# Kernel tuning notes

Measured on AMD Instinct MI355X. Metric: run time of the kernel, lower is better.

Reference implementation:

```python
import jax, jax.numpy as jnp
import numpy as np

B, C, N, H = 4, 256, 1024, 8
D = C            # per-head q/k dim (out_channels defaults to in_channels)
DV = C           # per-head value/output dim (y_out_channels defaults to out_channels)


def setup_inputs() -> dict:
    key = jax.random.key(0)
    ks = jax.random.split(key, 10)
    s = 0.02
    return {
        "x": jax.random.normal(ks[0], (B, C, N), jnp.float32),
        "y": jax.random.normal(ks[1], (B, C, N), jnp.float32),
        "Wq": jax.random.normal(ks[2], (H * D, C), jnp.float32) * s,
        "bq": jnp.zeros((H * D,), jnp.float32),
        "Wk": jax.random.normal(ks[3], (H * D, C), jnp.float32) * s,
        "bk": jnp.zeros((H * D,), jnp.float32),
        "Wv": jax.random.normal(ks[4], (H * DV, C), jnp.float32) * s,
        "bv": jnp.zeros((H * DV,), jnp.float32),
        "Wp": jax.random.normal(ks[5], (DV, C), jnp.float32) * s,  # projection, bias=False
        "gamma": jax.random.uniform(ks[6], (H, 1, 1, 1), jnp.float32) + 0.001,
    }


def _pconv(t, W, b):
    # 1x1 conv1d: (O,C) x (B,C,N) -> (B,O,N)
    out = jnp.einsum('oc,bcn->bon', W, t)
    return out if b is None else out + b[None, :, None]


def reference(x, y, Wq, bq, Wk, bk, Wv, bv, Wp, gamma):
    b_, _, n_ = x.shape
    h = gamma.shape[0]
    # Q/K/V projections, split channels into h heads (head-major chunks of D)
    q = _pconv(x, Wq, bq).reshape(b_, h, -1, n_)   # [B,H,D,N]
    k = _pconv(x, Wk, bk).reshape(b_, h, -1, n_)   # [B,H,D,N]
    v = _pconv(y, Wv, bv).reshape(b_, h, -1, n_)   # [B,H,DV,N]
    # energy[i,j] = sum_d q[d,i]*k[d,j]; softmax over keys j (no sqrt(d) scaling)
    attn = jax.nn.softmax(jnp.einsum('bhdn,bhdm->bhnm', q, k), axis=-1)
    out = jnp.einsum('bhdm,bhnm->bhdn', v, attn)   # [B,H,DV,N]
    # residual branch: y projected to DV channels (1x1 conv, no bias)
    yp = jnp.einsum('oc,bcn->bon', Wp, y)          # [B,DV,N]
    g = gamma.reshape(1, h, 1, 1)
    out = (g * out + yp[:, None, :, :]) / (1.0 + g)
    # concat heads along channel dim (head-major), matching split_cat(out,1,0,2)
    return out.reshape(b_, -1, n_)                 # [B,H*DV,N]
```

## Files before the change

### kernel.cpp

```cpp
#include <hip/hip_runtime.h>

#define Bb 4
#define Cc 256
#define Nn 1024
#define Hh 8
#define Oo 2048

typedef __attribute__((ext_vector_type(8))) short bf16x8;
typedef __attribute__((ext_vector_type(4))) float f32x4;

__device__ __forceinline__ short f2bf(float f) {
  unsigned u = __builtin_bit_cast(unsigned, f);
  unsigned r = u + 0x7FFFu + ((u >> 16) & 1u);
  return (short)(r >> 16);
}
__device__ __forceinline__ f32x4 mfma16(bf16x8 a, bf16x8 b, f32x4 c) {
  return __builtin_amdgcn_mfma_f32_16x16x32_bf16(a, b, c, 0, 0, 0);
}
__device__ __forceinline__ void gl_lds16(const void* g, void* l) {
  __builtin_amdgcn_global_load_lds(
      (const __attribute__((address_space(1))) void*)g,
      (__attribute__((address_space(3))) void*)l, 16, 0, 0);
}

__device__ __forceinline__ void stage_row512(const char* gbase, char* lds,
                                             int wave, int lane) {
#pragma unroll
  for (int i = 0; i < 8; i++) {
    int off = (wave * 8 + i) * 1024;
    int L = off + lane * 16;
    int r = L >> 9;
    int c = ((L >> 4) & 31) ^ (r & 7);
    gl_lds16(gbase + r * 512 + c * 16, lds + off);
  }
}
__device__ __forceinline__ void stage_v(const char* Vg, char* lds, int k0,
                                        int wave, int lane) {
#pragma unroll
  for (int i = 0; i < 8; i++) {
    int off = (wave * 8 + i) * 1024;
    int L = off + lane * 16;
    int r = L >> 7;
    int c = ((L >> 4) & 7) ^ (r & 7);
    gl_lds16(Vg + (size_t)r * 2048 + k0 * 2 + c * 16, lds + off);
  }
}

__global__ __launch_bounds__(256) void k_transpose(
    const float* __restrict__ x, const float* __restrict__ y,
    short* __restrict__ xT, short* __restrict__ yT,
    const float* __restrict__ Wq, const float* __restrict__ Wk,
    const float* __restrict__ Wv, const float* __restrict__ Wp,
    short* __restrict__ dWq, short* __restrict__ dWk, short* __restrict__ dWv,
    short* __restrict__ dWp) {
  {
    const int NW = Oo * Cc;
    int lin = blockIdx.x + 16 * (blockIdx.y + 4 * blockIdx.z);
    for (int i = (lin * 256 + threadIdx.x) * 4; i < 3 * NW + Cc * Cc;
         i += 512 * 256 * 4) {
      const float* src;
      short* dst;
      int off;
      if (i < NW) {
        src = Wq; dst = dWq; off = i;
      } else if (i < 2 * NW) {
        src = Wk; dst = dWk; off = i - NW;
      } else if (i < 3 * NW) {
        src = Wv; dst = dWv; off = i - 2 * NW;
      } else {
        src = Wp; dst = dWp; off = i - 3 * NW;
      }
      float4 v = *(const float4*)(src + off);
      short4 o;
      o.x = f2bf(v.x);
      o.y = f2bf(v.y);
      o.z = f2bf(v.z);
      o.w = f2bf(v.w);
      *(short4*)(dst + off) = o;
    }
  }
  int bz = blockIdx.z;
  int b = bz >> 1;
  const float* src = (bz & 1) ? y : x;
  short* dst = (bz & 1) ? yT : xT;
  src += (size_t)b * Cc * Nn;
  dst += (size_t)b * Nn * Cc;
  __shared__ short tile[64][72];
  int n0 = blockIdx.x * 64, c0 = blockIdx.y * 64;
  int t = threadIdx.x;
#pragma unroll
  for (int i = 0; i < 16; i++) {
    int idx = t + i * 256;
    int cc = idx >> 6, nn = idx & 63;
    tile[cc][nn] = f2bf(src[(size_t)(c0 + cc) * Nn + n0 + nn]);
  }
  __syncthreads();
#pragma unroll
  for (int i = 0; i < 16; i++) {
    int idx = t + i * 256;
    int nn = idx >> 6, cc = idx & 63;
    dst[(size_t)(n0 + nn) * Cc + c0 + cc] = tile[cc][nn];
  }
}

__global__ __launch_bounds__(256) void k_proj_qk(
    const short* __restrict__ xT, const short* __restrict__ Wq,
    const float* __restrict__ bq, const short* __restrict__ Wk,
    const float* __restrict__ bk, short* __restrict__ Qt,
    short* __restrict__ Kt) {
  int b = blockIdx.z, n0 = blockIdx.x * 64, o0 = blockIdx.y * 64;
  int wave = threadIdx.x >> 6, lane = threadIdx.x & 63;
  int quad = lane >> 4, l16 = lane & 15;
  int sw = l16 & 7;
  __shared__ short Wqs[64 * 256];
  __shared__ short Wks[64 * 256];

  stage_row512((const char*)(Wq + (size_t)o0 * Cc), (char*)Wqs, wave, lane);
  stage_row512((const char*)(Wk + (size_t)o0 * Cc), (char*)Wks, wave, lane);
  const short* aptr =
      xT + (size_t)b * Nn * Cc + (size_t)(n0 + wave * 16 + l16) * Cc + quad * 8;
  bf16x8 areg[8];
#pragma unroll
  for (int ks = 0; ks < 8; ks++) areg[ks] = *(const bf16x8*)(aptr + ks * 32);

  f32x4 accQ[4], accK[4];
#pragma unroll
  for (int j = 0; j < 4; j++) {
    accQ[j] = f32x4{0.f, 0.f, 0.f, 0.f};
    accK[j] = f32x4{0.f, 0.f, 0.f, 0.f};
  }
  __syncthreads();
#pragma unroll
  for (int ks = 0; ks < 8; ks++) {
#pragma unroll
    for (int cj = 0; cj < 4; cj++) {
      int off = (cj * 16 + l16) * 512 + (((ks * 4 + quad) ^ sw) << 4);
      bf16x8 wqf = *(const bf16x8*)((const char*)Wqs + off);
      bf16x8 wkf = *(const bf16x8*)((const char*)Wks + off);
      accQ[cj] = mfma16(areg[ks], wqf, accQ[cj]);
      accK[cj] = mfma16(areg[ks], wkf, accK[cj]);
    }
  }
#pragma unroll
  for (int cj = 0; cj < 4; cj++) {
    int o = o0 + cj * 16 + l16;
    int h = o >> 8, d = o & 255;
    float vbq = bq[o];
    float vbk = bk[o];
#pragma unroll
    for (int r = 0; r < 4; r++) {
      int n = n0 + wave * 16 + quad * 4 + r;
      size_t idx = (((size_t)(b * Hh + h) * Nn) + n) * 256 + d;
      Qt[idx] = f2bf(accQ[cj][r] + vbq);
      Kt[idx] = f2bf(accK[cj][r] + vbk);
    }
  }
}

__global__ __launch_bounds__(256) void k_proj_v(
    const short* __restrict__ yTs, const short* __restrict__ Wv,
    const float* __restrict__ bv, const short* __restrict__ Wp,
    short* __restrict__ Vv, float* __restrict__ yp) {
  int b = blockIdx.z, n0 = blockIdx.x * 64;
  int by = blockIdx.y;
  bool isP = by >= 32;
  const short* W = isP ? Wp : Wv;
  int o0 = (isP ? (by - 32) : by) * 64;
  int wave = threadIdx.x >> 6, lane = threadIdx.x & 63;
  int quad = lane >> 4, l16 = lane & 15;
  int sw = l16 & 7;
  __shared__ short Ys[64 * 256];

  stage_row512((const char*)(yTs + (size_t)b * Nn * Cc + (size_t)n0 * Cc),
               (char*)Ys, wave, lane);
  const short* aptr = W + (size_t)(o0 + wave * 16 + l16) * Cc + quad * 8;
  bf16x8 areg[8];
#pragma unroll
  for (int ks = 0; ks < 8; ks++) areg[ks] = *(const bf16x8*)(aptr + ks * 32);

  f32x4 acc[4];
#pragma unroll
  for (int j = 0; j < 4; j++) acc[j] = f32x4{0.f, 0.f, 0.f, 0.f};
  __syncthreads();
#pragma unroll
  for (int ks = 0; ks < 8; ks++) {
#pragma unroll
    for (int cj = 0; cj < 4; cj++) {
      bf16x8 bb = *(const bf16x8*)((const char*)Ys + (cj * 16 + l16) * 512 +
                                   (((ks * 4 + quad) ^ sw) << 4));
      acc[cj] = mfma16(areg[ks], bb, acc[cj]);
    }
  }
#pragma unroll
  for (int cj = 0; cj < 4; cj++) {
    int n = n0 + cj * 16 + l16;
#pragma unroll
    for (int r = 0; r < 4; r++) {
      int o = o0 + wave * 16 + quad * 4 + r;
      if (isP) {
        yp[((size_t)b * Cc + o) * Nn + n] = acc[cj][r];
      } else {
        float v = acc[cj][r] + bv[o];
        Vv[((size_t)b * Oo + o) * Nn + n] = f2bf(v);
      }
    }
  }
}

__global__ __launch_bounds__(256) void k_attn(
    const short* __restrict__ Qt, const short* __restrict__ Kt,
    const short* __restrict__ Vv, const float* __restrict__ yp,
    const float* __restrict__ gamma, float* __restrict__ out) {
  int id = blockIdx.x;
  int bh = (id & 7) * 4 + (id >> 7);
  int q0 = ((id >> 3) & 15) * 64;
  int b = bh >> 3, h = bh & 7;
  int wave = threadIdx.x >> 6, lane = threadIdx.x & 63;
  int quad = lane >> 4, l16 = lane & 15;
  int sw = l16 & 7;
  const short* Qb = Qt + (size_t)bh * Nn * 256;
  const char* Kg = (const char*)(Kt + (size_t)bh * Nn * 256);
  const char* Vg = (const char*)(Vv + (size_t)bh * 256 * Nn);

  __shared__ short Klds[64 * 256];
  __shared__ short Vlds[256 * 64];
  __shared__ short plds[4][16][64];
  __shared__ float llds[64];

  bf16x8 qreg[8];
  {
    const short* qp = Qb + (size_t)(q0 + wave * 16 + l16) * 256 + quad * 8;
#pragma unroll
    for (int ks = 0; ks < 8; ks++) qreg[ks] = *(const bf16x8*)(qp + ks * 32);
  }
  f32x4 oacc[16];
#pragma unroll
  for (int j = 0; j < 16; j++) oacc[j] = f32x4{0.f, 0.f, 0.f, 0.f};
  float l_i[4] = {0.f, 0.f, 0.f, 0.f};

  stage_row512(Kg, (char*)Klds, wave, lane);
  stage_v(Vg, (char*)Vlds, 0, wave, lane);

  for (int kt = 0; kt < 16; kt++) {
    int k0 = kt * 64;
    __syncthreads();
    f32x4 sc[4];
#pragma unroll
    for (int j = 0; j < 4; j++) sc[j] = f32x4{0.f, 0.f, 0.f, 0.f};
#pragma unroll
    for (int ks = 0; ks < 8; ks++) {
#pragma unroll
      for (int cj = 0; cj < 4; cj++) {
        bf16x8 kb = *(const bf16x8*)((const char*)Klds +
                                     (cj * 16 + l16) * 512 +
                                     (((ks * 4 + quad) ^ sw) << 4));
        sc[cj] = mfma16(qreg[ks], kb, sc[cj]);
      }
    }
#pragma unroll
    for (int cj = 0; cj < 4; cj++) {
#pragma unroll
      for (int r = 0; r < 4; r++) {
        float p = __expf(sc[cj][r]);
        l_i[r] += p;
        int row = quad * 4 + r;
        plds[wave][row][(((cj * 2 + (l16 >> 3)) ^ (row & 7)) << 3) | sw] =
            f2bf(p);
      }
    }
    __syncthreads();
    if (kt < 15)
      stage_row512(Kg + (size_t)(k0 + 64) * 512, (char*)Klds, wave, lane);
    bf16x8 ap0[4], ap1[4];
#pragma unroll
    for (int qb = 0; qb < 4; qb++) {
      ap0[qb] = *(const bf16x8*)&plds[qb][l16][(quad ^ sw) << 3];
      ap1[qb] = *(const bf16x8*)&plds[qb][l16][((quad + 4) ^ sw) << 3];
    }
#pragma unroll
    for (int dj = 0; dj < 4; dj++) {
      const char* vrow = (const char*)Vlds + (wave * 64 + dj * 16 + l16) * 128;
      bf16x8 v0 = *(const bf16x8*)(vrow + ((quad ^ sw) << 4));
      bf16x8 v1 = *(const bf16x8*)(vrow + (((quad + 4) ^ sw) << 4));
#pragma unroll
      for (int qb = 0; qb < 4; qb++) {
        oacc[qb * 4 + dj] = mfma16(ap0[qb], v0, oacc[qb * 4 + dj]);
        oacc[qb * 4 + dj] = mfma16(ap1[qb], v1, oacc[qb * 4 + dj]);
      }
    }
    __syncthreads();
    if (kt < 15) stage_v(Vg, (char*)Vlds, k0 + 64, wave, lane);
  }
#pragma unroll
  for (int r = 0; r < 4; r++) {
    float v = l_i[r];
    v += __shfl_xor(v, 1);
    v += __shfl_xor(v, 2);
    v += __shfl_xor(v, 4);
    v += __shfl_xor(v, 8);
    l_i[r] = v;
  }
  if (l16 == 0) {
    f32x4 lv;
#pragma unroll
    for (int r = 0; r < 4; r++) lv[r] = l_i[r];
    *(f32x4*)&llds[wave * 16 + quad * 4] = lv;
  }
  __syncthreads();
  float gf = gamma[h];
  float sg = gf / (1.f + gf), sy = 1.f / (1.f + gf);
#pragma unroll
  for (int qb = 0; qb < 4; qb++) {
    f32x4 lv = *(const f32x4*)&llds[qb * 16 + quad * 4];
    int qq = q0 + qb * 16 + quad * 4;
#pragma unroll
    for (int dj = 0; dj < 4; dj++) {
      int dv = wave * 64 + dj * 16 + l16;
      const float* ypp = yp + ((size_t)b * 256 + dv) * Nn + qq;
      float* op = out + ((size_t)b * Oo + h * 256 + dv) * Nn + qq;
      float4 yv = *(const float4*)ypp;
      f32x4 oa = oacc[qb * 4 + dj];
      float4 ov;
      ov.x = sg * (oa[0] / lv[0]) + sy * yv.x;
      ov.y = sg * (oa[1] / lv[1]) + sy * yv.y;
      ov.z = sg * (oa[2] / lv[2]) + sy * yv.z;
      ov.w = sg * (oa[3] / lv[3]) + sy * yv.w;
      *(float4*)op = ov;
    }
  }
}

extern "C" void kernel_launch(void* const* d_in, const int* in_sizes, int n_in,
                              void* d_out, int out_size, void* d_ws,
                              size_t ws_size, hipStream_t stream) {
  const float* x = (const float*)d_in[0];
  const float* y = (const float*)d_in[1];
  const float* Wq = (const float*)d_in[2];
  const float* bq = (const float*)d_in[3];
  const float* Wk = (const float*)d_in[4];
  const float* bk = (const float*)d_in[5];
  const float* Wv = (const float*)d_in[6];
  const float* bv = (const float*)d_in[7];
  const float* Wp = (const float*)d_in[8];
  const float* gamma = (const float*)d_in[9];
  float* out = (float*)d_out;

  char* w = (char*)d_ws;
  short* Qt = (short*)(w + 0);
  short* Kt = (short*)(w + 16777216);
  short* Vv = (short*)(w + 33554432);
  short* xT = (short*)(w + 50331648);
  short* yT = (short*)(w + 52428800);
  float* yp = (float*)(w + 54525952);
  short* Wqb = (short*)(w + 58720256);
  short* Wkb = (short*)(w + 59768832);
  short* Wvb = (short*)(w + 60817408);
  short* Wpb = (short*)(w + 61865984);

  k_transpose<<<dim3(Nn / 64, Cc / 64, 2 * Bb), dim3(256), 0, stream>>>(
      x, y, xT, yT, Wq, Wk, Wv, Wp, Wqb, Wkb, Wvb, Wpb);
  k_proj_qk<<<dim3(Nn / 64, Oo / 64, Bb), dim3(256), 0, stream>>>(
      xT, Wqb, bq, Wkb, bk, Qt, Kt);
  k_proj_v<<<dim3(Nn / 64, 36, Bb), dim3(256), 0, stream>>>(yT, Wvb, bv, Wpb,
                                                            Vv, yp);
  k_attn<<<dim3(512), dim3(256), 0, stream>>>(Qt, Kt, Vv, yp, gamma, out);
}
```

Baseline: 183.2 us.

## Vectorize Q/K projection stores and hand-tune attention barriers with partial waitcnt

The Q/K projection swaps the MFMA operands so each lane holds four consecutive output channels, which lets it store Q/K as short4 vectors and load the biases as float4. The attention loop replaces __syncthreads with explicit s_barrier plus partial vmcnt/lgkmcnt waits, sched barriers and s_setprio around the MFMA blocks. The goal is to let the asynchronous K/V global-to-LDS loads overlap with compute instead of being drained at every barrier. The hand-written vmcnt(8) count depends on how many loads are in flight; if that count is wrong, LDS data could be read before it has arrived.

```diff
diff --git a/kernel.cpp b/kernel.cpp
--- a/kernel.cpp
+++ b/kernel.cpp
@@ -137,23 +137,29 @@
       int off = (cj * 16 + l16) * 512 + (((ks * 4 + quad) ^ sw) << 4);
       bf16x8 wqf = *(const bf16x8*)((const char*)Wqs + off);
       bf16x8 wkf = *(const bf16x8*)((const char*)Wks + off);
-      accQ[cj] = mfma16(areg[ks], wqf, accQ[cj]);
-      accK[cj] = mfma16(areg[ks], wkf, accK[cj]);
+      accQ[cj] = mfma16(wqf, areg[ks], accQ[cj]);
+      accK[cj] = mfma16(wkf, areg[ks], accK[cj]);
     }
   }
 #pragma unroll
   for (int cj = 0; cj < 4; cj++) {
-    int o = o0 + cj * 16 + l16;
-    int h = o >> 8, d = o & 255;
-    float vbq = bq[o];
-    float vbk = bk[o];
-#pragma unroll
-    for (int r = 0; r < 4; r++) {
-      int n = n0 + wave * 16 + quad * 4 + r;
-      size_t idx = (((size_t)(b * Hh + h) * Nn) + n) * 256 + d;
-      Qt[idx] = f2bf(accQ[cj][r] + vbq);
-      Kt[idx] = f2bf(accK[cj][r] + vbk);
-    }
+    int obase = o0 + cj * 16 + quad * 4;
+    int h = obase >> 8, d = obase & 255;
+    int n = n0 + wave * 16 + l16;
+    float4 vbq = *(const float4*)(bq + obase);
+    float4 vbk = *(const float4*)(bk + obase);
+    size_t idx = (((size_t)(b * Hh + h) * Nn) + n) * 256 + d;
+    short4 oq, ok;
+    oq.x = f2bf(accQ[cj][0] + vbq.x);
+    oq.y = f2bf(accQ[cj][1] + vbq.y);
+    oq.z = f2bf(accQ[cj][2] + vbq.z);
+    oq.w = f2bf(accQ[cj][3] + vbq.w);
+    ok.x = f2bf(accK[cj][0] + vbk.x);
+    ok.y = f2bf(accK[cj][1] + vbk.y);
+    ok.z = f2bf(accK[cj][2] + vbk.z);
+    ok.w = f2bf(accK[cj][3] + vbk.w);
+    *(short4*)(Qt + idx) = oq;
+    *(short4*)(Kt + idx) = ok;
   }
 }
 
@@ -243,10 +249,13 @@
 
   for (int kt = 0; kt < 16; kt++) {
     int k0 = kt * 64;
-    __syncthreads();
+    asm volatile("s_waitcnt vmcnt(8)" ::: "memory");
+    __builtin_amdgcn_s_barrier();
+    __builtin_amdgcn_sched_barrier(0);
     f32x4 sc[4];
 #pragma unroll
     for (int j = 0; j < 4; j++) sc[j] = f32x4{0.f, 0.f, 0.f, 0.f};
+    __builtin_amdgcn_s_setprio(1);
 #pragma unroll
     for (int ks = 0; ks < 8; ks++) {
 #pragma unroll
@@ -257,6 +266,7 @@
         sc[cj] = mfma16(qreg[ks], kb, sc[cj]);
       }
     }
+    __builtin_amdgcn_s_setprio(0);
 #pragma unroll
     for (int cj = 0; cj < 4; cj++) {
 #pragma unroll
@@ -268,7 +278,9 @@
             f2bf(p);
       }
     }
-    __syncthreads();
+    asm volatile("s_waitcnt vmcnt(0) lgkmcnt(0)" ::: "memory");
+    __builtin_amdgcn_s_barrier();
+    __builtin_amdgcn_sched_barrier(0);
     if (kt < 15)
       stage_row512(Kg + (size_t)(k0 + 64) * 512, (char*)Klds, wave, lane);
     bf16x8 ap0[4], ap1[4];
@@ -277,6 +289,7 @@
       ap0[qb] = *(const bf16x8*)&plds[qb][l16][(quad ^ sw) << 3];
       ap1[qb] = *(const bf16x8*)&plds[qb][l16][((quad + 4) ^ sw) << 3];
     }
+    __builtin_amdgcn_s_setprio(1);
 #pragma unroll
     for (int dj = 0; dj < 4; dj++) {
       const char* vrow = (const char*)Vlds + (wave * 64 + dj * 16 + l16) * 128;
@@ -288,7 +301,10 @@
         oacc[qb * 4 + dj] = mfma16(ap1[qb], v1, oacc[qb * 4 + dj]);
       }
     }
-    __syncthreads();
+    __builtin_amdgcn_s_setprio(0);
+    asm volatile("s_waitcnt lgkmcnt(0)" ::: "memory");
+    __builtin_amdgcn_s_barrier();
+    __builtin_amdgcn_sched_barrier(0);
     if (kt < 15) stage_v(Vg, (char*)Vlds, k0 + 64, wave, lane);
   }
 #pragma unroll
```

Measured after the change: 211.6 us. 1.15x slower.

## Merge Q/K/V/P projection kernels and vectorize transpose and Q/K stores

Applied to the files above, without the earlier changes.

Combines the separate Q/K and V/P projection kernels into one launch with 100 y-blocks, where each block picks Q, K, V or P and uses a single 32 KB LDS tile. This drops one launch and halves LDS per block, allowing more blocks per CU. For Q/K the MFMA operands are swapped so each lane writes four contiguous d values as a short4 with a float4 bias load. The transpose kernel now reads with float4 loads and writes short4 stores. The single-LDS design stages the Q/K weight tile once per projection instead of sharing it across Q and K, so weight staging traffic roughly doubles.

```diff
diff --git a/kernel.cpp b/kernel.cpp
--- a/kernel.cpp
+++ b/kernel.cpp
@@ -85,123 +85,113 @@
   short* dst = (bz & 1) ? yT : xT;
   src += (size_t)b * Cc * Nn;
   dst += (size_t)b * Nn * Cc;
-  __shared__ short tile[64][72];
+  __shared__ short tile[64][68];
   int n0 = blockIdx.x * 64, c0 = blockIdx.y * 64;
   int t = threadIdx.x;
 #pragma unroll
-  for (int i = 0; i < 16; i++) {
+  for (int i = 0; i < 4; i++) {
     int idx = t + i * 256;
-    int cc = idx >> 6, nn = idx & 63;
-    tile[cc][nn] = f2bf(src[(size_t)(c0 + cc) * Nn + n0 + nn]);
+    int cc = idx >> 4, ng = idx & 15;
+    float4 v = *(const float4*)(src + (size_t)(c0 + cc) * Nn + n0 + ng * 4);
+    short4 o;
+    o.x = f2bf(v.x);
+    o.y = f2bf(v.y);
+    o.z = f2bf(v.z);
+    o.w = f2bf(v.w);
+    *(short4*)&tile[cc][ng * 4] = o;
   }
   __syncthreads();
 #pragma unroll
-  for (int i = 0; i < 16; i++) {
+  for (int i = 0; i < 4; i++) {
     int idx = t + i * 256;
-    int nn = idx >> 6, cc = idx & 63;
-    dst[(size_t)(n0 + nn) * Cc + c0 + cc] = tile[cc][nn];
-  }
-}
-
-__global__ __launch_bounds__(256) void k_proj_qk(
-    const short* __restrict__ xT, const short* __restrict__ Wq,
-    const float* __restrict__ bq, const short* __restrict__ Wk,
-    const float* __restrict__ bk, short* __restrict__ Qt,
-    short* __restrict__ Kt) {
-  int b = blockIdx.z, n0 = blockIdx.x * 64, o0 = blockIdx.y * 64;
+    int nn = idx >> 4, c4 = idx & 15;
+    short4 o;
+    o.x = tile[c4 * 4 + 0][nn];
+    o.y = tile[c4 * 4 + 1][nn];
+    o.z = tile[c4 * 4 + 2][nn];
+    o.w = tile[c4 * 4 + 3][nn];
+    *(short4*)(dst + (size_t)(n0 + nn) * Cc + c0 + c4 * 4) = o;
+  }
+}
+
+__global__ __launch_bounds__(256, 4) void k_proj(
+    const short* __restrict__ xT, const short* __restrict__ yT,
+    const short* __restrict__ Wqb, const float* __restrict__ bq,
+    const short* __restrict__ Wkb, const float* __restrict__ bk,
+    const short* __restrict__ Wvb, const float* __restrict__ bv,
+    const short* __restrict__ Wpb, short* __restrict__ Qt,
+    short* __restrict__ Kt, short* __restrict__ Vv, float* __restrict__ yp) {
+  int b = blockIdx.z, n0 = blockIdx.x * 64;
+  int yb = blockIdx.y;
+  int path = yb >> 5;
+  int o0 = (yb & 31) * 64;
+  const short* W = path == 0 ? Wqb : path == 1 ? Wkb : path == 2 ? Wvb : Wpb;
+  bool dataStaged = path >= 2;
   int wave = threadIdx.x >> 6, lane = threadIdx.x & 63;
   int quad = lane >> 4, l16 = lane & 15;
   int sw = l16 & 7;
-  __shared__ short Wqs[64 * 256];
-  __shared__ short Wks[64 * 256];
-
-  stage_row512((const char*)(Wq + (size_t)o0 * Cc), (char*)Wqs, wave, lane);
-  stage_row512((const char*)(Wk + (size_t)o0 * Cc), (char*)Wks, wave, lane);
+  __shared__ short Ws[64 * 256];
+
+  const char* stage_src =
+      dataStaged ? (const char*)(yT + (size_t)b * Nn * Cc + (size_t)n0 * Cc)
+                 : (const char*)(W + (size_t)o0 * Cc);
+  stage_row512(stage_src, (char*)Ws, wave, lane);
+
   const short* aptr =
-      xT + (size_t)b * Nn * Cc + (size_t)(n0 + wave * 16 + l16) * Cc + quad * 8;
+      dataStaged
+          ? W + (size_t)(o0 + wave * 16 + l16) * Cc + quad * 8
+          : xT + (size_t)b * Nn * Cc + (size_t)(n0 + wave * 16 + l16) * Cc +
+                quad * 8;
   bf16x8 areg[8];
 #pragma unroll
   for (int ks = 0; ks < 8; ks++) areg[ks] = *(const bf16x8*)(aptr + ks * 32);
 
-  f32x4 accQ[4], accK[4];
-#pragma unroll
-  for (int j = 0; j < 4; j++) {
-    accQ[j] = f32x4{0.f, 0.f, 0.f, 0.f};
-    accK[j] = f32x4{0.f, 0.f, 0.f, 0.f};
-  }
+  f32x4 acc[4];
+#pragma unroll
+  for (int j = 0; j < 4; j++) acc[j] = f32x4{0.f, 0.f, 0.f, 0.f};
   __syncthreads();
 #pragma unroll
   for (int ks = 0; ks < 8; ks++) {
 #pragma unroll
     for (int cj = 0; cj < 4; cj++) {
       int off = (cj * 16 + l16) * 512 + (((ks * 4 + quad) ^ sw) << 4);
-      bf16x8 wqf = *(const bf16x8*)((const char*)Wqs + off);
-      bf16x8 wkf = *(const bf16x8*)((const char*)Wks + off);
-      accQ[cj] = mfma16(areg[ks], wqf, accQ[cj]);
-      accK[cj] = mfma16(areg[ks], wkf, accK[cj]);
-    }
-  }
-#pragma unroll
-  for (int cj = 0; cj < 4; cj++) {
-    int o = o0 + cj * 16 + l16;
-    int h = o >> 8, d = o & 255;
-    float vbq = bq[o];
-    float vbk = bk[o];
-#pragma unroll
-    for (int r = 0; r < 4; r++) {
-      int n = n0 + wave * 16 + quad * 4 + r;
+      bf16x8 wf = *(const bf16x8*)((const char*)Ws + off);
+      if (dataStaged)
+        acc[cj] = mfma16(areg[ks], wf, acc[cj]);
+      else
+        acc[cj] = mfma16(wf, areg[ks], acc[cj]);
+    }
+  }
+  if (path < 2) {
+    short* Od = path == 0 ? Qt : Kt;
+    const float* bias = path == 0 ? bq : bk;
+#pragma unroll
+    for (int cj = 0; cj < 4; cj++) {
+      int obase = o0 + cj * 16 + quad * 4;
+      int h = obase >> 8, d = obase & 255;
+      int n = n0 + wave * 16 + l16;
+      float4 vb = *(const float4*)(bias + obase);
       size_t idx = (((size_t)(b * Hh + h) * Nn) + n) * 256 + d;
-      Qt[idx] = f2bf(accQ[cj][r] + vbq);
-      Kt[idx] = f2bf(accK[cj][r] + vbk);
-    }
-  }
-}
-
-__global__ __launch_bounds__(256) void k_proj_v(
-    const short* __restrict__ yTs, const short* __restrict__ Wv,
-    const float* __restrict__ bv, const short* __restrict__ Wp,
-    short* __restrict__ Vv, float* __restrict__ yp) {
-  int b = blockIdx.z, n0 = blockIdx.x * 64;
-  int by = blockIdx.y;
-  bool isP = by >= 32;
-  const short* W = isP ? Wp : Wv;
-  int o0 = (isP ? (by - 32) : by) * 64;
-  int wave = threadIdx.x >> 6, lane = threadIdx.x & 63;
-  int quad = lane >> 4, l16 = lane & 15;
-  int sw = l16 & 7;
-  __shared__ short Ys[64 * 256];
-
-  stage_row512((const char*)(yTs + (size_t)b * Nn * Cc + (size_t)n0 * Cc),
-               (char*)Ys, wave, lane);
-  const short* aptr = W + (size_t)(o0 + wave * 16 + l16) * Cc + quad * 8;
-  bf16x8 areg[8];
-#pragma unroll
-  for (int ks = 0; ks < 8; ks++) areg[ks] = *(const bf16x8*)(aptr + ks * 32);
-
-  f32x4 acc[4];
-#pragma unroll
-  for (int j = 0; j < 4; j++) acc[j] = f32x4{0.f, 0.f, 0.f, 0.f};
-  __syncthreads();
-#pragma unroll
-  for (int ks = 0; ks < 8; ks++) {
+      short4 o;
+      o.x = f2bf(acc[cj][0] + vb.x);
+      o.y = f2bf(acc[cj][1] + vb.y);
+      o.z = f2bf(acc[cj][2] + vb.z);
+      o.w = f2bf(acc[cj][3] + vb.w);
+      *(short4*)(Od + idx) = o;
+    }
+  } else {
 #pragma unroll
     for (int cj = 0; cj < 4; cj++) {
-      bf16x8 bb = *(const bf16x8*)((const char*)Ys + (cj * 16 + l16) * 512 +
-                                   (((ks * 4 + quad) ^ sw) << 4));
-      acc[cj] = mfma16(areg[ks], bb, acc[cj]);
-    }
-  }
-#pragma unroll
-  for (int cj = 0; cj < 4; cj++) {
-    int n = n0 + cj * 16 + l16;
-#pragma unroll
-    for (int r = 0; r < 4; r++) {
-      int o = o0 + wave * 16 + quad * 4 + r;
-      if (isP) {
-        yp[((size_t)b * Cc + o) * Nn + n] = acc[cj][r];
-      } else {
-        float v = acc[cj][r] + bv[o];
-        Vv[((size_t)b * Oo + o) * Nn + n] = f2bf(v);
+      int n = n0 + cj * 16 + l16;
+#pragma unroll
+      for (int r = 0; r < 4; r++) {
+        int o = o0 + wave * 16 + quad * 4 + r;
+        if (path == 3) {
+          yp[((size_t)b * Cc + o) * Nn + n] = acc[cj][r];
+        } else {
+          float v = acc[cj][r] + bv[o];
+          Vv[((size_t)b * Oo + o) * Nn + n] = f2bf(v);
+        }
       }
     }
   }
@@ -359,9 +349,7 @@
 
   k_transpose<<<dim3(Nn / 64, Cc / 64, 2 * Bb), dim3(256), 0, stream>>>(
       x, y, xT, yT, Wq, Wk, Wv, Wp, Wqb, Wkb, Wvb, Wpb);
-  k_proj_qk<<<dim3(Nn / 64, Oo / 64, Bb), dim3(256), 0, stream>>>(
-      xT, Wqb, bq, Wkb, bk, Qt, Kt);
-  k_proj_v<<<dim3(Nn / 64, 36, Bb), dim3(256), 0, stream>>>(yT, Wvb, bv, Wpb,
-                                                            Vv, yp);
+  k_proj<<<dim3(Nn / 64, 100, Bb), dim3(256), 0, stream>>>(
+      xT, yT, Wqb, bq, Wkb, bk, Wvb, bv, Wpb, Qt, Kt, Vv, yp);
   k_attn<<<dim3(512), dim3(256), 0, stream>>>(Qt, Kt, Vv, yp, gamma, out);
 }
```

Result: slower. 189.5 us (+3.4%).
